# Optimization experiments

Hardware: AMD Instinct MI355X
Metric: run time of the kernel (lower is better)

The kernel has to match this reference:

```python
import jax, jax.numpy as jnp
import numpy as np

L, D, H, HD, FF, V, NH, S = 5, 1024, 8, 128, 4096, 2048, 15, 2
EPS = 1e-6
THETA = 10000.0


def rms_norm(x, w):
    x32 = x.astype(jnp.float32)
    y = x32 * jax.lax.rsqrt(jnp.mean(x32 * x32, axis=-1, keepdims=True) + EPS)
    return (y * w.astype(jnp.float32)).astype(x.dtype)


def rotate_half(x):
    x1, x2 = x[..., : HD // 2], x[..., HD // 2:]
    return jnp.concatenate((-x2, x1), axis=-1)


def setup_inputs() -> dict:
    key = jax.random.key(0)
    ks = jax.random.split(key, 20)
    s = 0.02
    inp = {
        "past_hidden": jax.random.normal(ks[0], (1, 1, D), jnp.float32),
        "cb0_token": jax.random.randint(ks[1], (1, 1), 0, V, jnp.int32),
        "codec_emb": jax.random.normal(ks[2], (V, D), jnp.float32) * s,
        "Wq": jax.random.normal(ks[3], (L, D, H * HD), jnp.float32) * s,
        "Wk": jax.random.normal(ks[4], (L, D, H * HD), jnp.float32) * s,
        "Wv": jax.random.normal(ks[5], (L, D, H * HD), jnp.float32) * s,
        "Wo": jax.random.normal(ks[6], (L, H * HD, D), jnp.float32) * s,
        "q_norm_w": jnp.ones((L, HD), jnp.float32),
        "k_norm_w": jnp.ones((L, HD), jnp.float32),
        "ln1_w": jnp.ones((L, D), jnp.float32),
        "ln2_w": jnp.ones((L, D), jnp.float32),
        "Wgate": jax.random.normal(ks[7], (L, D, FF), jnp.float32) * s,
        "Wup": jax.random.normal(ks[8], (L, D, FF), jnp.float32) * s,
        "Wdown": jax.random.normal(ks[9], (L, FF, D), jnp.float32) * s,
        "final_norm_w": jnp.ones((D,), jnp.float32),
        "lm_heads": jax.random.normal(ks[10], (NH, D, V), jnp.float32) * s,
    }
    return inp


def reference(past_hidden, codec_emb, Wq, Wk, Wv, Wo, q_norm_w, k_norm_w,
              ln1_w, ln2_w, Wgate, Wup, Wdown, final_norm_w, lm_heads,
              cb0_token):
    # Embed CB0 token and build 2-token prefill sequence [1, 2, D].
    cb0_embed = codec_emb[cb0_token]            # [1, 1, D]
    h = jnp.concatenate([past_hidden, cb0_embed], axis=1)

    # Rotary cos/sin for positions [0, 1]: [1, 1, S, HD].
    pos = jnp.arange(S, dtype=jnp.float32)
    inv_freq = 1.0 / (THETA ** (jnp.arange(0, HD, 2, dtype=jnp.float32) / HD))
    freqs = pos[:, None] * inv_freq[None, :]    # [S, HD/2]
    emb = jnp.concatenate([freqs, freqs], axis=-1)
    cos = jnp.cos(emb)[None, None]
    sin = jnp.sin(emb)[None, None]

    causal_mask = jnp.array([[0.0, -1e9], [0.0, 0.0]], jnp.float32)
    scale = 1.0 / np.sqrt(HD)

    def layer_step(h, p):
        wq, wk, wv, wo, qn, kn, l1, l2, wg, wu, wd = p
        res = h
        x = rms_norm(h, l1)                     # [1, S, D]
        q = (x @ wq).reshape(1, S, H, HD)
        k = (x @ wk).reshape(1, S, H, HD)
        v = (x @ wv).reshape(1, S, H, HD)
        q = rms_norm(q, qn)                     # per-head qk-norm
        k = rms_norm(k, kn)
        q = q.transpose(0, 2, 1, 3)             # [1, H, S, HD]
        k = k.transpose(0, 2, 1, 3)
        v = v.transpose(0, 2, 1, 3)
        q = q * cos + rotate_half(q) * sin
        k = k * cos + rotate_half(k) * sin
        attn = jnp.einsum('bhqd,bhkd->bhqk', q, k) * scale + causal_mask
        w = jax.nn.softmax(attn.astype(jnp.float32), axis=-1).astype(q.dtype)
        o = jnp.einsum('bhqk,bhkd->bhqd', w, v)
        o = o.transpose(0, 2, 1, 3).reshape(1, S, H * HD) @ wo
        h = res + o
        res = h
        x = rms_norm(h, l2)
        mlp = (jax.nn.silu(x @ wg) * (x @ wu)) @ wd
        return res + mlp, (k, v)

    h, (ks_, vs_) = jax.lax.scan(
        layer_step, h,
        (Wq, Wk, Wv, Wo, q_norm_w, k_norm_w, ln1_w, ln2_w, Wgate, Wup, Wdown))

    h = rms_norm(h, final_norm_w)
    last = h[:, -1, :]                          # [1, D]
    all_logits = jnp.einsum('bd,ndv->nbv', last, lm_heads)  # [15, 1, V]
    # Interleave keys/values per layer: [2L, 1, H, S, HD].
    kv_cache = jnp.stack([ks_, vs_], axis=1).reshape(2 * L, 1, H, S, HD)
    return all_logits, kv_cache
```

## Files before the change

### kernel.cpp

```cpp
#include <hip/hip_runtime.h>
#include <math.h>

#define EPS 1e-6f


__global__ void init_kernel(const float* __restrict__ past_hidden,
                            const float* __restrict__ codec_emb,
                            const int* __restrict__ tok,
                            float* __restrict__ ws,
                            float* __restrict__ logits)
{
    size_t idx = (size_t)blockIdx.x * blockDim.x + threadIdx.x;
    size_t stride = (size_t)gridDim.x * blockDim.x;
    for (size_t i = idx; i < 30720; i += stride) ws[2048 + i] = 0.f;
    for (size_t i = idx; i < 81920; i += stride) ws[43008 + i] = 0.f;
    for (size_t i = idx; i < 30720; i += stride) logits[i] = 0.f;
    int t = tok[0];
    for (size_t i = idx; i < 1024; i += stride) {
        ws[i]        = past_hidden[i];
        ws[1024 + i] = codec_emb[(size_t)t * 1024 + i];
    }
}

template <int S>
__global__ __launch_bounds__(256) void gemv_rms(
    const float* __restrict__ hbuf,
    const float* __restrict__ nw,
    const float* __restrict__ W0,
    const float* __restrict__ W1,
    const float* __restrict__ W2,
    size_t w_zstride,
    float* __restrict__ out,
    int out_sstride, int out_zstride,
    int D, int N)
{
    __shared__ float xs[S * 1024];
    __shared__ float red[S * 1024];
    __shared__ float tot[S];
    const int t = threadIdx.x;

    const float* W;
    if (W1) W = (blockIdx.z == 0) ? W0 : ((blockIdx.z == 1) ? W1 : W2);
    else    W = W0 + (size_t)blockIdx.z * w_zstride;
    float* outz = out + (size_t)blockIdx.z * out_zstride;

    if (nw) {
        float ss[S];
#pragma unroll
        for (int s = 0; s < S; ++s) ss[s] = 0.f;
        for (int dd = t; dd < D; dd += 256) {
#pragma unroll
            for (int s = 0; s < S; ++s) {
                float v = hbuf[s * D + dd];
                xs[s * 1024 + dd] = v;
                ss[s] += v * v;
            }
        }
#pragma unroll
        for (int s = 0; s < S; ++s) {
            red[t] = ss[s]; __syncthreads();
            for (int off = 128; off >= 1; off >>= 1) {
                if (t < off) red[t] += red[t + off];
                __syncthreads();
            }
            if (t == 0) tot[s] = red[0];
            __syncthreads();
        }
        float sc[S];
#pragma unroll
        for (int s = 0; s < S; ++s) sc[s] = rsqrtf(tot[s] / (float)D + EPS);
        for (int dd = t; dd < D; dd += 256) {
            float wv = nw[dd];
#pragma unroll
            for (int s = 0; s < S; ++s)
                xs[s * 1024 + dd] = xs[s * 1024 + dd] * sc[s] * wv;
        }
        __syncthreads();
    } else {
        for (int dd = t; dd < D; dd += 256) {
#pragma unroll
            for (int s = 0; s < S; ++s) xs[s * 1024 + dd] = hbuf[s * D + dd];
        }
        __syncthreads();
    }

    const int lane = t & 63;
    const int dp = t >> 6;
    const int j = blockIdx.x * 256 + lane * 4;
    const int d0 = blockIdx.y * 64 + dp * 16;

    float acc[S][4];
#pragma unroll
    for (int s = 0; s < S; ++s) { acc[s][0] = acc[s][1] = acc[s][2] = acc[s][3] = 0.f; }
#pragma unroll
    for (int i = 0; i < 16; ++i) {
        int dd = d0 + i;
        float4 w4 = *reinterpret_cast<const float4*>(W + (size_t)dd * N + j);
#pragma unroll
        for (int s = 0; s < S; ++s) {
            float xv = xs[s * 1024 + dd];
            acc[s][0] += xv * w4.x; acc[s][1] += xv * w4.y;
            acc[s][2] += xv * w4.z; acc[s][3] += xv * w4.w;
        }
    }
    __syncthreads();
#pragma unroll
    for (int s = 0; s < S; ++s)
#pragma unroll
        for (int c = 0; c < 4; ++c)
            red[(dp * S + s) * 256 + lane * 4 + c] = acc[s][c];
    __syncthreads();
    for (int o = t; o < S * 256; o += 256) {
        int s = o >> 8;
        int col = o & 255;
        float sum = 0.f;
#pragma unroll
        for (int dp2 = 0; dp2 < 4; ++dp2) sum += red[(dp2 * S + s) * 256 + col];
        atomicAdd(outz + (size_t)s * out_sstride + blockIdx.x * 256 + col, sum);
    }
}

__global__ void attn_kernel(const float* __restrict__ qkv,
                            const float* __restrict__ qnw,
                            const float* __restrict__ knw,
                            float* __restrict__ ao,
                            float* __restrict__ kvc)
{
    const int h = blockIdx.x;
    const int d = threadIdx.x;
    __shared__ float rbuf[128];
    __shared__ float qb[2][128], kb[2][128];

    float q[2], k[2], v[2];
#pragma unroll
    for (int s = 0; s < 2; ++s) {
        q[s] = qkv[s * 3072 +        h * 128 + d];
        k[s] = qkv[s * 3072 + 1024 + h * 128 + d];
        v[s] = qkv[s * 3072 + 2048 + h * 128 + d];
    }
    auto bred = [&](float val) -> float {
        rbuf[d] = val; __syncthreads();
        for (int off = 64; off >= 1; off >>= 1) {
            if (d < off) rbuf[d] += rbuf[d + off];
            __syncthreads();
        }
        float r = rbuf[0]; __syncthreads();
        return r;
    };
    float qs0 = bred(q[0] * q[0]);
    float qs1 = bred(q[1] * q[1]);
    float ks0 = bred(k[0] * k[0]);
    float ks1 = bred(k[1] * k[1]);
    float qsc[2] = { rsqrtf(qs0 / 128.f + EPS), rsqrtf(qs1 / 128.f + EPS) };
    float ksc[2] = { rsqrtf(ks0 / 128.f + EPS), rsqrtf(ks1 / 128.f + EPS) };
#pragma unroll
    for (int s = 0; s < 2; ++s) {
        qb[s][d] = q[s] * qsc[s] * qnw[d];
        kb[s][d] = k[s] * ksc[s] * knw[d];
    }
    __syncthreads();
    float invf = powf(10000.f, -(float)(d & 63) / 64.f);
    float qr[2], kr[2];
#pragma unroll
    for (int s = 0; s < 2; ++s) {
        float ang = (float)s * invf;
        float c = cosf(ang), si = sinf(ang);
        float qrot = (d < 64) ? -qb[s][d + 64] : qb[s][d - 64];
        float krot = (d < 64) ? -kb[s][d + 64] : kb[s][d - 64];
        qr[s] = qb[s][d] * c + qrot * si;
        kr[s] = kb[s][d] * c + krot * si;
    }
#pragma unroll
    for (int s = 0; s < 2; ++s) {
        kvc[h * 256 + s * 128 + d]        = kr[s];
        kvc[2048 + h * 256 + s * 128 + d] = v[s];
    }
    float p00 = bred(qr[0] * kr[0]);
    float p01 = bred(qr[0] * kr[1]);
    float p10 = bred(qr[1] * kr[0]);
    float p11 = bred(qr[1] * kr[1]);
    const float scale = 0.08838834764831845f;
    float s00 = p00 * scale, s01 = p01 * scale - 1e9f;
    float m0 = fmaxf(s00, s01);
    float e0 = expf(s00 - m0), e1 = expf(s01 - m0);
    float in0 = 1.f / (e0 + e1);
    float w00 = e0 * in0, w01 = e1 * in0;
    float s10 = p10 * scale, s11 = p11 * scale;
    float m1 = fmaxf(s10, s11);
    float f0 = expf(s10 - m1), f1 = expf(s11 - m1);
    float in1 = 1.f / (f0 + f1);
    float w10 = f0 * in1, w11 = f1 * in1;

    ao[0 * 1024 + h * 128 + d] = w00 * v[0] + w01 * v[1];
    ao[1 * 1024 + h * 128 + d] = w10 * v[0] + w11 * v[1];
}

__global__ __launch_bounds__(256) void gemv_down(
    const float* __restrict__ gu,
    const float* __restrict__ W,
    float* __restrict__ out)
{
    __shared__ float a[2][64];
    __shared__ float red[2048];
    const int t = threadIdx.x;
    const int d0 = blockIdx.y * 64;
    if (t < 128) {
        int s = t >> 6, f = d0 + (t & 63);
        float g = gu[s * 8192 + f];
        float u = gu[s * 8192 + 4096 + f];
        float sg = g / (1.f + expf(-g));
        a[s][t & 63] = sg * u;
    }
    __syncthreads();
    const int lane = t & 63;
    const int dp = t >> 6;
    const int j = blockIdx.x * 256 + lane * 4;
    float acc[2][4] = {{0.f,0.f,0.f,0.f},{0.f,0.f,0.f,0.f}};
#pragma unroll
    for (int i = 0; i < 16; ++i) {
        int dl = dp * 16 + i;
        int dd = d0 + dl;
        float4 w4 = *reinterpret_cast<const float4*>(W + (size_t)dd * 1024 + j);
#pragma unroll
        for (int s = 0; s < 2; ++s) {
            float xv = a[s][dl];
            acc[s][0] += xv * w4.x; acc[s][1] += xv * w4.y;
            acc[s][2] += xv * w4.z; acc[s][3] += xv * w4.w;
        }
    }
#pragma unroll
    for (int s = 0; s < 2; ++s)
#pragma unroll
        for (int c = 0; c < 4; ++c)
            red[(dp * 2 + s) * 256 + lane * 4 + c] = acc[s][c];
    __syncthreads();
    for (int o = t; o < 512; o += 256) {
        int s = o >> 8, col = o & 255;
        float sum = 0.f;
#pragma unroll
        for (int dp2 = 0; dp2 < 4; ++dp2) sum += red[(dp2 * 2 + s) * 256 + col];
        atomicAdd(out + s * 1024 + blockIdx.x * 256 + col, sum);
    }
}

__global__ void final_norm_kernel(const float* __restrict__ h,
                                  const float* __restrict__ w,
                                  float* __restrict__ outx)
{
    __shared__ float rbuf[256];
    __shared__ float tot;
    int t = threadIdx.x;
    float ss = 0.f;
    for (int dd = t; dd < 1024; dd += 256) { float v = h[1024 + dd]; ss += v * v; }
    rbuf[t] = ss; __syncthreads();
    for (int off = 128; off >= 1; off >>= 1) {
        if (t < off) rbuf[t] += rbuf[t + off];
        __syncthreads();
    }
    if (t == 0) tot = rbuf[0];
    __syncthreads();
    float sc = rsqrtf(tot / 1024.f + EPS);
    for (int dd = t; dd < 1024; dd += 256) outx[dd] = h[1024 + dd] * sc * w[dd];
}

extern "C" void kernel_launch(void* const* d_in, const int* in_sizes, int n_in,
                              void* d_out, int out_size, void* d_ws, size_t ws_size,
                              hipStream_t stream)
{
    const float* past_hidden = (const float*)d_in[0];
    const int*   cb0         = (const int*)d_in[1];
    const float* codec_emb   = (const float*)d_in[2];
    const float* Wq  = (const float*)d_in[3];
    const float* Wk  = (const float*)d_in[4];
    const float* Wv  = (const float*)d_in[5];
    const float* Wo  = (const float*)d_in[6];
    const float* qnw = (const float*)d_in[7];
    const float* knw = (const float*)d_in[8];
    const float* ln1 = (const float*)d_in[9];
    const float* ln2 = (const float*)d_in[10];
    const float* Wg  = (const float*)d_in[11];
    const float* Wu  = (const float*)d_in[12];
    const float* Wd  = (const float*)d_in[13];
    const float* fnw = (const float*)d_in[14];
    const float* lmh = (const float*)d_in[15];

    float* out = (float*)d_out;
    float* ws  = (float*)d_ws;
    float* h      = ws;
    float* qkvb   = ws + 2048;
    float* aob    = ws + 32768;
    float* gub    = ws + 43008;
    float* lastn  = ws + 124928;
    float* logits = out;
    float* kvc    = out + 30720;

    init_kernel<<<256, 256, 0, stream>>>(past_hidden, codec_emb, cb0, ws, logits);

    for (int l = 0; l < 5; ++l) {
        const float* wq = Wq + (size_t)l * 1024 * 1024;
        const float* wk = Wk + (size_t)l * 1024 * 1024;
        const float* wv = Wv + (size_t)l * 1024 * 1024;
        const float* wo = Wo + (size_t)l * 1024 * 1024;
        const float* wg = Wg + (size_t)l * 1024 * 4096;
        const float* wu = Wu + (size_t)l * 1024 * 4096;
        const float* wd = Wd + (size_t)l * 4096 * 1024;
        float* qkv = qkvb + (size_t)l * 6144;
        float* ao  = aob  + (size_t)l * 2048;
        float* gu  = gub  + (size_t)l * 16384;

        gemv_rms<2><<<dim3(4, 16, 3), 256, 0, stream>>>(
            h, ln1 + l * 1024, wq, wk, wv, 0, qkv, 3072, 1024, 1024, 1024);
        attn_kernel<<<8, 128, 0, stream>>>(qkv, qnw + l * 128, knw + l * 128, ao,
                                           kvc + (size_t)(2 * l) * 2048);
        gemv_rms<2><<<dim3(4, 16, 1), 256, 0, stream>>>(
            ao, nullptr, wo, nullptr, nullptr, 0, h, 1024, 0, 1024, 1024);
        gemv_rms<2><<<dim3(16, 16, 2), 256, 0, stream>>>(
            h, ln2 + l * 1024, wg, wu, wu, 0, gu, 8192, 4096, 1024, 4096);
        gemv_down<<<dim3(4, 64), 256, 0, stream>>>(gu, wd, h);
    }

    final_norm_kernel<<<1, 256, 0, stream>>>(h, fnw, lastn);
    gemv_rms<1><<<dim3(8, 16, 15), 256, 0, stream>>>(
        lastn, nullptr, lmh, nullptr, nullptr, (size_t)1024 * 2048,
        logits, 2048, 2048, 1024, 2048);
}
```

Measured before the change: 537.8 us.

## Fuse all layers into one persistent kernel with grid barriers and weight prefetch

Replaces the per-layer chain of separate kernel launches with a single persistent kernel of 256 workgroups that walks every layer stage, separated by atomic-counter grid barriers. Idle workgroups touch upcoming weight tiles to warm the cache while other stages run, and the attention step now writes into a zeroed buffer with atomics. This removes launch gaps and tail idle time, but relies on all 256 workgroups being co-resident and adds spin-barrier cost plus redundant prefetch loads.

```diff
diff --git a/kernel.cpp b/kernel.cpp
--- a/kernel.cpp
+++ b/kernel.cpp
@@ -2,7 +2,13 @@
 #include <math.h>
 
 #define EPS 1e-6f
-
+#define NWG 256
+
+#define WS_H    0
+#define WS_QKV  2048
+#define WS_AO   32768
+#define WS_GU   43008
+#define WS_CNT  126976
 
 __global__ void init_kernel(const float* __restrict__ past_hidden,
                             const float* __restrict__ codec_emb,
@@ -10,175 +16,193 @@
                             float* __restrict__ ws,
                             float* __restrict__ logits)
 {
-    size_t idx = (size_t)blockIdx.x * blockDim.x + threadIdx.x;
-    size_t stride = (size_t)gridDim.x * blockDim.x;
-    for (size_t i = idx; i < 30720; i += stride) ws[2048 + i] = 0.f;
-    for (size_t i = idx; i < 81920; i += stride) ws[43008 + i] = 0.f;
-    for (size_t i = idx; i < 30720; i += stride) logits[i] = 0.f;
+    int idx = blockIdx.x * blockDim.x + threadIdx.x;
+    int stride = gridDim.x * blockDim.x;
+    for (int i = idx; i < 30720; i += stride) ws[WS_QKV + i] = 0.f;
+    for (int i = idx; i < 10240; i += stride) ws[WS_AO + i] = 0.f;
+    for (int i = idx; i < 81920; i += stride) ws[WS_GU + i] = 0.f;
+    for (int i = idx; i < 30720; i += stride) logits[i] = 0.f;
+    for (int i = idx; i < 64; i += stride) ((unsigned*)(ws + WS_CNT))[i] = 0u;
     int t = tok[0];
-    for (size_t i = idx; i < 1024; i += stride) {
+    for (int i = idx; i < 1024; i += stride) {
         ws[i]        = past_hidden[i];
         ws[1024 + i] = codec_emb[(size_t)t * 1024 + i];
     }
 }
 
+__device__ __forceinline__ void gbar(unsigned* cnt, unsigned target)
+{
+    __threadfence();
+    __syncthreads();
+    if (threadIdx.x == 0) {
+        __hip_atomic_fetch_add(cnt, 1u, __ATOMIC_ACQ_REL, __HIP_MEMORY_SCOPE_AGENT);
+        while (__hip_atomic_load(cnt, __ATOMIC_RELAXED, __HIP_MEMORY_SCOPE_AGENT) < target) {
+            __builtin_amdgcn_s_sleep(2);
+        }
+    }
+    __syncthreads();
+    __threadfence();
+}
+
+__device__ __forceinline__ float wave_red64(float v)
+{
+    for (int o = 32; o >= 1; o >>= 1) v += __shfl_down(v, o, 64);
+    return v;
+}
+
+__device__ __forceinline__ void load_rms2(const float* __restrict__ h,
+                                          const float* __restrict__ nw,
+                                          float* __restrict__ x0, float* __restrict__ x1,
+                                          float* __restrict__ red)
+{
+    int t = threadIdx.x;
+    float ss0 = 0.f, ss1 = 0.f;
+    for (int d = t; d < 1024; d += 256) {
+        float v0 = h[d], v1 = h[1024 + d];
+        x0[d] = v0; x1[d] = v1;
+        ss0 += v0 * v0; ss1 += v1 * v1;
+    }
+    ss0 = wave_red64(ss0); ss1 = wave_red64(ss1);
+    if ((t & 63) == 0) { red[t >> 6] = ss0; red[4 + (t >> 6)] = ss1; }
+    __syncthreads();
+    float s0 = red[0] + red[1] + red[2] + red[3];
+    float s1 = red[4] + red[5] + red[6] + red[7];
+    float sc0 = rsqrtf(s0 / 1024.f + EPS);
+    float sc1 = rsqrtf(s1 / 1024.f + EPS);
+    __syncthreads();
+    for (int d = t; d < 1024; d += 256) {
+        float w = nw[d];
+        x0[d] *= sc0 * w; x1[d] *= sc1 * w;
+    }
+    __syncthreads();
+}
+
+__device__ __forceinline__ void load_rms1(const float* __restrict__ hrow,
+                                          const float* __restrict__ nw,
+                                          float* __restrict__ x,
+                                          float* __restrict__ red)
+{
+    int t = threadIdx.x;
+    float ss = 0.f;
+    for (int d = t; d < 1024; d += 256) { float v = hrow[d]; x[d] = v; ss += v * v; }
+    ss = wave_red64(ss);
+    if ((t & 63) == 0) red[t >> 6] = ss;
+    __syncthreads();
+    float s = red[0] + red[1] + red[2] + red[3];
+    float sc = rsqrtf(s / 1024.f + EPS);
+    __syncthreads();
+    for (int d = t; d < 1024; d += 256) x[d] *= sc * nw[d];
+    __syncthreads();
+}
+
 template <int S>
-__global__ __launch_bounds__(256) void gemv_rms(
-    const float* __restrict__ hbuf,
-    const float* __restrict__ nw,
-    const float* __restrict__ W0,
-    const float* __restrict__ W1,
-    const float* __restrict__ W2,
-    size_t w_zstride,
-    float* __restrict__ out,
-    int out_sstride, int out_zstride,
-    int D, int N)
-{
-    __shared__ float xs[S * 1024];
-    __shared__ float red[S * 1024];
-    __shared__ float tot[S];
-    const int t = threadIdx.x;
-
-    const float* W;
-    if (W1) W = (blockIdx.z == 0) ? W0 : ((blockIdx.z == 1) ? W1 : W2);
-    else    W = W0 + (size_t)blockIdx.z * w_zstride;
-    float* outz = out + (size_t)blockIdx.z * out_zstride;
-
-    if (nw) {
-        float ss[S];
-#pragma unroll
-        for (int s = 0; s < S; ++s) ss[s] = 0.f;
-        for (int dd = t; dd < D; dd += 256) {
-#pragma unroll
-            for (int s = 0; s < S; ++s) {
-                float v = hbuf[s * D + dd];
-                xs[s * 1024 + dd] = v;
-                ss[s] += v * v;
-            }
-        }
-#pragma unroll
-        for (int s = 0; s < S; ++s) {
-            red[t] = ss[s]; __syncthreads();
-            for (int off = 128; off >= 1; off >>= 1) {
-                if (t < off) red[t] += red[t + off];
-                __syncthreads();
-            }
-            if (t == 0) tot[s] = red[0];
-            __syncthreads();
-        }
-        float sc[S];
-#pragma unroll
-        for (int s = 0; s < S; ++s) sc[s] = rsqrtf(tot[s] / (float)D + EPS);
-        for (int dd = t; dd < D; dd += 256) {
-            float wv = nw[dd];
-#pragma unroll
-            for (int s = 0; s < S; ++s)
-                xs[s * 1024 + dd] = xs[s * 1024 + dd] * sc[s] * wv;
-        }
-        __syncthreads();
-    } else {
-        for (int dd = t; dd < D; dd += 256) {
-#pragma unroll
-            for (int s = 0; s < S; ++s) xs[s * 1024 + dd] = hbuf[s * D + dd];
-        }
-        __syncthreads();
-    }
-
-    const int lane = t & 63;
-    const int dp = t >> 6;
-    const int j = blockIdx.x * 256 + lane * 4;
-    const int d0 = blockIdx.y * 64 + dp * 16;
-
-    float acc[S][4];
-#pragma unroll
-    for (int s = 0; s < S; ++s) { acc[s][0] = acc[s][1] = acc[s][2] = acc[s][3] = 0.f; }
+__device__ __forceinline__ void task_gemm(const float* __restrict__ x0,
+                                          const float* __restrict__ x1,
+                                          const float* __restrict__ Wt, int N,
+                                          float* __restrict__ o0, float* __restrict__ o1,
+                                          float* __restrict__ red)
+{
+    const int t = threadIdx.x, lane = t & 63, dp = t >> 6;
+    const float* Wp = Wt + (size_t)(dp * 16) * N + lane * 4;
+    const float* xa = x0 + dp * 16;
+    const float* xb = (S == 2) ? (x1 + dp * 16) : nullptr;
+    float a0 = 0.f, a1 = 0.f, a2 = 0.f, a3 = 0.f;
+    float b0 = 0.f, b1 = 0.f, b2 = 0.f, b3 = 0.f;
 #pragma unroll
     for (int i = 0; i < 16; ++i) {
-        int dd = d0 + i;
-        float4 w4 = *reinterpret_cast<const float4*>(W + (size_t)dd * N + j);
+        float4 w = *reinterpret_cast<const float4*>(Wp + (size_t)i * N);
+        float xv = xa[i];
+        a0 += xv * w.x; a1 += xv * w.y; a2 += xv * w.z; a3 += xv * w.w;
+        if (S == 2) {
+            float yv = xb[i];
+            b0 += yv * w.x; b1 += yv * w.y; b2 += yv * w.z; b3 += yv * w.w;
+        }
+    }
+    __syncthreads();
+    red[(dp * S + 0) * 256 + lane * 4 + 0] = a0;
+    red[(dp * S + 0) * 256 + lane * 4 + 1] = a1;
+    red[(dp * S + 0) * 256 + lane * 4 + 2] = a2;
+    red[(dp * S + 0) * 256 + lane * 4 + 3] = a3;
+    if (S == 2) {
+        red[(dp * S + 1) * 256 + lane * 4 + 0] = b0;
+        red[(dp * S + 1) * 256 + lane * 4 + 1] = b1;
+        red[(dp * S + 1) * 256 + lane * 4 + 2] = b2;
+        red[(dp * S + 1) * 256 + lane * 4 + 3] = b3;
+    }
+    __syncthreads();
+    for (int o = t; o < S * 256; o += 256) {
+        int s = o >> 8, col = o & 255;
+        float sum = red[(0 * S + s) * 256 + col] + red[(1 * S + s) * 256 + col]
+                  + red[(2 * S + s) * 256 + col] + red[(3 * S + s) * 256 + col];
+        atomicAdd(((s == 0) ? o0 : o1) + col, sum);
+    }
+}
+
+__device__ __forceinline__ float touch_tile(const float* __restrict__ Wt, int N)
+{
+    const int t = threadIdx.x, lane = t & 63, dp = t >> 6;
+    const float* Wp = Wt + (size_t)(dp * 16) * N + lane * 4;
+    float s = 0.f;
 #pragma unroll
-        for (int s = 0; s < S; ++s) {
-            float xv = xs[s * 1024 + dd];
-            acc[s][0] += xv * w4.x; acc[s][1] += xv * w4.y;
-            acc[s][2] += xv * w4.z; acc[s][3] += xv * w4.w;
-        }
-    }
-    __syncthreads();
-#pragma unroll
-    for (int s = 0; s < S; ++s)
-#pragma unroll
-        for (int c = 0; c < 4; ++c)
-            red[(dp * S + s) * 256 + lane * 4 + c] = acc[s][c];
-    __syncthreads();
-    for (int o = t; o < S * 256; o += 256) {
-        int s = o >> 8;
-        int col = o & 255;
-        float sum = 0.f;
-#pragma unroll
-        for (int dp2 = 0; dp2 < 4; ++dp2) sum += red[(dp2 * S + s) * 256 + col];
-        atomicAdd(outz + (size_t)s * out_sstride + blockIdx.x * 256 + col, sum);
-    }
-}
-
-__global__ void attn_kernel(const float* __restrict__ qkv,
-                            const float* __restrict__ qnw,
-                            const float* __restrict__ knw,
-                            float* __restrict__ ao,
-                            float* __restrict__ kvc)
-{
-    const int h = blockIdx.x;
-    const int d = threadIdx.x;
-    __shared__ float rbuf[128];
-    __shared__ float qb[2][128], kb[2][128];
-
-    float q[2], k[2], v[2];
-#pragma unroll
-    for (int s = 0; s < 2; ++s) {
-        q[s] = qkv[s * 3072 +        h * 128 + d];
-        k[s] = qkv[s * 3072 + 1024 + h * 128 + d];
-        v[s] = qkv[s * 3072 + 2048 + h * 128 + d];
+    for (int i = 0; i < 16; ++i) {
+        float4 w = *reinterpret_cast<const float4*>(Wp + (size_t)i * N);
+        s += w.x + w.y + w.z + w.w;
+    }
+    return s;
+}
+
+__device__ void attn_head(const float* __restrict__ qkv,
+                          const float* __restrict__ qnw, const float* __restrict__ knw,
+                          float* __restrict__ ao, float* __restrict__ kvc,
+                          int head, float* __restrict__ red)
+{
+    const int t = threadIdx.x;
+    const int d = t & 127;
+    const bool act = t < 128;
+    float q0 = 0.f, q1 = 0.f, k0 = 0.f, k1 = 0.f, v0 = 0.f, v1 = 0.f, qw = 0.f, kw = 0.f;
+    if (act) {
+        q0 = qkv[head * 128 + d];           q1 = qkv[3072 + head * 128 + d];
+        k0 = qkv[1024 + head * 128 + d];    k1 = qkv[3072 + 1024 + head * 128 + d];
+        v0 = qkv[2048 + head * 128 + d];    v1 = qkv[3072 + 2048 + head * 128 + d];
+        qw = qnw[d]; kw = knw[d];
     }
     auto bred = [&](float val) -> float {
-        rbuf[d] = val; __syncthreads();
-        for (int off = 64; off >= 1; off >>= 1) {
-            if (d < off) rbuf[d] += rbuf[d + off];
+        red[t] = act ? val : 0.f; __syncthreads();
+        for (int off = 128; off >= 1; off >>= 1) {
+            if (t < off) red[t] += red[t + off];
             __syncthreads();
         }
-        float r = rbuf[0]; __syncthreads();
+        float r = red[0]; __syncthreads();
         return r;
     };
-    float qs0 = bred(q[0] * q[0]);
-    float qs1 = bred(q[1] * q[1]);
-    float ks0 = bred(k[0] * k[0]);
-    float ks1 = bred(k[1] * k[1]);
-    float qsc[2] = { rsqrtf(qs0 / 128.f + EPS), rsqrtf(qs1 / 128.f + EPS) };
-    float ksc[2] = { rsqrtf(ks0 / 128.f + EPS), rsqrtf(ks1 / 128.f + EPS) };
-#pragma unroll
-    for (int s = 0; s < 2; ++s) {
-        qb[s][d] = q[s] * qsc[s] * qnw[d];
-        kb[s][d] = k[s] * ksc[s] * knw[d];
-    }
-    __syncthreads();
-    float invf = powf(10000.f, -(float)(d & 63) / 64.f);
-    float qr[2], kr[2];
-#pragma unroll
-    for (int s = 0; s < 2; ++s) {
-        float ang = (float)s * invf;
-        float c = cosf(ang), si = sinf(ang);
-        float qrot = (d < 64) ? -qb[s][d + 64] : qb[s][d - 64];
-        float krot = (d < 64) ? -kb[s][d + 64] : kb[s][d - 64];
-        qr[s] = qb[s][d] * c + qrot * si;
-        kr[s] = kb[s][d] * c + krot * si;
-    }
-#pragma unroll
-    for (int s = 0; s < 2; ++s) {
-        kvc[h * 256 + s * 128 + d]        = kr[s];
-        kvc[2048 + h * 256 + s * 128 + d] = v[s];
-    }
-    float p00 = bred(qr[0] * kr[0]);
-    float p01 = bred(qr[0] * kr[1]);
-    float p10 = bred(qr[1] * kr[0]);
-    float p11 = bred(qr[1] * kr[1]);
+    float qs0 = bred(q0 * q0), qs1 = bred(q1 * q1);
+    float ks0 = bred(k0 * k0), ks1 = bred(k1 * k1);
+    float qsc0 = rsqrtf(qs0 / 128.f + EPS), qsc1 = rsqrtf(qs1 / 128.f + EPS);
+    float ksc0 = rsqrtf(ks0 / 128.f + EPS), ksc1 = rsqrtf(ks1 / 128.f + EPS);
+    float* qb = red + 256;
+    float* kb = red + 512;
+    if (act) {
+        qb[d] = q0 * qsc0 * qw; qb[128 + d] = q1 * qsc1 * qw;
+        kb[d] = k0 * ksc0 * kw; kb[128 + d] = k1 * ksc1 * kw;
+    }
+    __syncthreads();
+    float qr0 = 0.f, qr1 = 0.f, kr0 = 0.f, kr1 = 0.f;
+    if (act) {
+        float invf = powf(10000.f, -(float)(d & 63) / 64.f);
+        qr0 = qb[d];
+        kr0 = kb[d];
+        float c = cosf(invf), si = sinf(invf);
+        float qrot = (d < 64) ? -qb[128 + d + 64] : qb[128 + d - 64];
+        float krot = (d < 64) ? -kb[128 + d + 64] : kb[128 + d - 64];
+        qr1 = qb[128 + d] * c + qrot * si;
+        kr1 = kb[128 + d] * c + krot * si;
+        kvc[head * 256 + d]              = kr0;
+        kvc[head * 256 + 128 + d]        = kr1;
+        kvc[2048 + head * 256 + d]       = v0;
+        kvc[2048 + head * 256 + 128 + d] = v1;
+    }
+    float p00 = bred(qr0 * kr0), p01 = bred(qr0 * kr1);
+    float p10 = bred(qr1 * kr0), p11 = bred(qr1 * kr1);
     const float scale = 0.08838834764831845f;
     float s00 = p00 * scale, s01 = p01 * scale - 1e9f;
     float m0 = fmaxf(s00, s01);
@@ -190,77 +214,145 @@
     float f0 = expf(s10 - m1), f1 = expf(s11 - m1);
     float in1 = 1.f / (f0 + f1);
     float w10 = f0 * in1, w11 = f1 * in1;
-
-    ao[0 * 1024 + h * 128 + d] = w00 * v[0] + w01 * v[1];
-    ao[1 * 1024 + h * 128 + d] = w10 * v[0] + w11 * v[1];
-}
-
-__global__ __launch_bounds__(256) void gemv_down(
-    const float* __restrict__ gu,
-    const float* __restrict__ W,
-    float* __restrict__ out)
-{
-    __shared__ float a[2][64];
+    if (act) {
+        atomicAdd(ao + head * 128 + d,        w00 * v0 + w01 * v1);
+        atomicAdd(ao + 1024 + head * 128 + d, w10 * v0 + w11 * v1);
+    }
+}
+
+__global__ __launch_bounds__(256) void mega_kernel(
+    const float* __restrict__ Wq, const float* __restrict__ Wk, const float* __restrict__ Wv,
+    const float* __restrict__ Wo,
+    const float* __restrict__ qnw_all, const float* __restrict__ knw_all,
+    const float* __restrict__ ln1_all, const float* __restrict__ ln2_all,
+    const float* __restrict__ Wg, const float* __restrict__ Wu, const float* __restrict__ Wd,
+    const float* __restrict__ fnw, const float* __restrict__ lmh,
+    float* __restrict__ ws, float* __restrict__ logits, float* __restrict__ kvc_all)
+{
+    __shared__ float xs0[1024];
+    __shared__ float xs1[1024];
     __shared__ float red[2048];
-    const int t = threadIdx.x;
-    const int d0 = blockIdx.y * 64;
-    if (t < 128) {
-        int s = t >> 6, f = d0 + (t & 63);
-        float g = gu[s * 8192 + f];
-        float u = gu[s * 8192 + 4096 + f];
-        float sg = g / (1.f + expf(-g));
-        a[s][t & 63] = sg * u;
-    }
-    __syncthreads();
-    const int lane = t & 63;
-    const int dp = t >> 6;
-    const int j = blockIdx.x * 256 + lane * 4;
-    float acc[2][4] = {{0.f,0.f,0.f,0.f},{0.f,0.f,0.f,0.f}};
-#pragma unroll
-    for (int i = 0; i < 16; ++i) {
-        int dl = dp * 16 + i;
-        int dd = d0 + dl;
-        float4 w4 = *reinterpret_cast<const float4*>(W + (size_t)dd * 1024 + j);
-#pragma unroll
-        for (int s = 0; s < 2; ++s) {
-            float xv = a[s][dl];
-            acc[s][0] += xv * w4.x; acc[s][1] += xv * w4.y;
-            acc[s][2] += xv * w4.z; acc[s][3] += xv * w4.w;
-        }
-    }
-#pragma unroll
-    for (int s = 0; s < 2; ++s)
-#pragma unroll
-        for (int c = 0; c < 4; ++c)
-            red[(dp * 2 + s) * 256 + lane * 4 + c] = acc[s][c];
-    __syncthreads();
-    for (int o = t; o < 512; o += 256) {
-        int s = o >> 8, col = o & 255;
-        float sum = 0.f;
-#pragma unroll
-        for (int dp2 = 0; dp2 < 4; ++dp2) sum += red[(dp2 * 2 + s) * 256 + col];
-        atomicAdd(out + s * 1024 + blockIdx.x * 256 + col, sum);
-    }
-}
-
-__global__ void final_norm_kernel(const float* __restrict__ h,
-                                  const float* __restrict__ w,
-                                  float* __restrict__ outx)
-{
-    __shared__ float rbuf[256];
-    __shared__ float tot;
-    int t = threadIdx.x;
-    float ss = 0.f;
-    for (int dd = t; dd < 1024; dd += 256) { float v = h[1024 + dd]; ss += v * v; }
-    rbuf[t] = ss; __syncthreads();
-    for (int off = 128; off >= 1; off >>= 1) {
-        if (t < off) rbuf[t] += rbuf[t + off];
-        __syncthreads();
-    }
-    if (t == 0) tot = rbuf[0];
-    __syncthreads();
-    float sc = rsqrtf(tot / 1024.f + EPS);
-    for (int dd = t; dd < 1024; dd += 256) outx[dd] = h[1024 + dd] * sc * w[dd];
+    const int wg = blockIdx.x;
+    unsigned* cnt = (unsigned*)(ws + WS_CNT);
+    unsigned target = 0;
+    float* h = ws + WS_H;
+    float sink = 0.f;
+
+    for (int l = 0; l < 5; ++l) {
+        const float* wq_ = Wq + (size_t)l * 1048576;
+        const float* wk_ = Wk + (size_t)l * 1048576;
+        const float* wv_ = Wv + (size_t)l * 1048576;
+        const float* wo_ = Wo + (size_t)l * 1048576;
+        const float* wg_ = Wg + (size_t)l * 4194304;
+        const float* wu_ = Wu + (size_t)l * 4194304;
+        const float* wd_ = Wd + (size_t)l * 4194304;
+        float* qkv = ws + WS_QKV + l * 6144;
+        float* ao  = ws + WS_AO  + l * 2048;
+        float* gu  = ws + WS_GU  + l * 16384;
+
+        load_rms2(h, ln1_all + l * 1024, xs0, xs1, red);
+        if (wg < 192) {
+            int z = wg >> 6, r = wg & 63, jb = r >> 4, kb = r & 15;
+            const float* Wz = (z == 0) ? wq_ : ((z == 1) ? wk_ : wv_);
+            task_gemm<2>(&xs0[kb * 64], &xs1[kb * 64],
+                         Wz + (size_t)(kb * 64) * 1024 + jb * 256, 1024,
+                         qkv + z * 1024 + jb * 256, qkv + 3072 + z * 1024 + jb * 256, red);
+        }
+        if (wg < 64) {
+            int jb = wg >> 4, kb = wg & 15;
+            sink += touch_tile(wo_ + (size_t)(kb * 64) * 1024 + jb * 256, 1024);
+        } else {
+            int jb = wg >> 4, kb = wg & 15;
+            sink += touch_tile(wg_ + (size_t)(kb * 64) * 4096 + jb * 256, 4096);
+        }
+        target += NWG; gbar(cnt, target);
+
+        if (wg < 8)
+            attn_head(qkv, qnw_all + l * 128, knw_all + l * 128, ao,
+                      kvc_all + (size_t)(2 * l) * 2048, wg, red);
+        if (wg < 64) {
+            int jb = wg >> 4, kb = wg & 15;
+            sink += touch_tile(wg_ + (size_t)(kb * 64) * 4096 + jb * 256, 4096);
+        }
+        target += NWG; gbar(cnt, target);
+
+        {
+            int t = threadIdx.x;
+            for (int d2 = t; d2 < 1024; d2 += 256) { xs0[d2] = ao[d2]; xs1[d2] = ao[1024 + d2]; }
+            __syncthreads();
+        }
+        if (wg < 64) {
+            int jb = wg >> 4, kb = wg & 15;
+            task_gemm<2>(&xs0[kb * 64], &xs1[kb * 64],
+                         wo_ + (size_t)(kb * 64) * 1024 + jb * 256, 1024,
+                         h + jb * 256, h + 1024 + jb * 256, red);
+        }
+        {
+            int jb = wg >> 4, kb = wg & 15;
+            sink += touch_tile(wu_ + (size_t)(kb * 64) * 4096 + jb * 256, 4096);
+        }
+        target += NWG; gbar(cnt, target);
+
+        load_rms2(h, ln2_all + l * 1024, xs0, xs1, red);
+        {
+            int jb = wg >> 4, kb = wg & 15;
+            task_gemm<2>(&xs0[kb * 64], &xs1[kb * 64],
+                         wg_ + (size_t)(kb * 64) * 4096 + jb * 256, 4096,
+                         gu + jb * 256, gu + 8192 + jb * 256, red);
+            task_gemm<2>(&xs0[kb * 64], &xs1[kb * 64],
+                         wu_ + (size_t)(kb * 64) * 4096 + jb * 256, 4096,
+                         gu + 4096 + jb * 256, gu + 8192 + 4096 + jb * 256, red);
+            int jb2 = wg >> 6, kb2 = wg & 63;
+            sink += touch_tile(wd_ + (size_t)(kb2 * 64) * 1024 + jb2 * 256, 1024);
+        }
+        target += NWG; gbar(cnt, target);
+
+        {
+            int jb = wg >> 6, kb = wg & 63;
+            int t = threadIdx.x;
+            if (t < 128) {
+                int s = t >> 6, f = kb * 64 + (t & 63);
+                float g = gu[s * 8192 + f];
+                float u = gu[s * 8192 + 4096 + f];
+                xs0[t & 63 + 0] = 0.f;
+            }
+            __syncthreads();
+            if (t < 128) {
+                int s = t >> 6, f = kb * 64 + (t & 63);
+                float g = gu[s * 8192 + f];
+                float u = gu[s * 8192 + 4096 + f];
+                float a = (g / (1.f + expf(-g))) * u;
+                if (s == 0) xs0[t & 63] = a; else xs1[t & 63] = a;
+            }
+            __syncthreads();
+            task_gemm<2>(&xs0[0], &xs1[0],
+                         wd_ + (size_t)(kb * 64) * 1024 + jb * 256, 1024,
+                         h + jb * 256, h + 1024 + jb * 256, red);
+            if (l < 4) {
+                if (wg < 192) {
+                    int z = wg >> 6, r = wg & 63, jb3 = r >> 4, kb3 = r & 15;
+                    const float* nq = (z == 0) ? (Wq + (size_t)(l + 1) * 1048576)
+                                   : ((z == 1) ? (Wk + (size_t)(l + 1) * 1048576)
+                                               : (Wv + (size_t)(l + 1) * 1048576));
+                    sink += touch_tile(nq + (size_t)(kb3 * 64) * 1024 + jb3 * 256, 1024);
+                }
+            } else {
+                int n = wg >> 7, r = wg & 127, jb3 = r >> 4, kb3 = r & 15;
+                sink += touch_tile(lmh + (size_t)n * 2097152 + (size_t)(kb3 * 64) * 2048 + jb3 * 256, 2048);
+            }
+        }
+        target += NWG; gbar(cnt, target);
+    }
+
+    load_rms1(h + 1024, fnw, xs0, red);
+    for (int task = wg; task < 1920; task += NWG) {
+        int n = task >> 7, r = task & 127, jb = r >> 4, kb = r & 15;
+        task_gemm<1>(&xs0[kb * 64], nullptr,
+                     lmh + (size_t)n * 2097152 + (size_t)(kb * 64) * 2048 + jb * 256, 2048,
+                     logits + n * 2048 + jb * 256, nullptr, red);
+    }
+
+    if (sink == -1.2345e38f) atomicAdd(h, 1.0f);
 }
 
 extern "C" void kernel_launch(void* const* d_in, const int* in_sizes, int n_in,
@@ -284,43 +376,12 @@
     const float* fnw = (const float*)d_in[14];
     const float* lmh = (const float*)d_in[15];
 
-    float* out = (float*)d_out;
-    float* ws  = (float*)d_ws;
-    float* h      = ws;
-    float* qkvb   = ws + 2048;
-    float* aob    = ws + 32768;
-    float* gub    = ws + 43008;
-    float* lastn  = ws + 124928;
+    float* out    = (float*)d_out;
+    float* ws     = (float*)d_ws;
     float* logits = out;
     float* kvc    = out + 30720;
 
-    init_kernel<<<256, 256, 0, stream>>>(past_hidden, codec_emb, cb0, ws, logits);
-
-    for (int l = 0; l < 5; ++l) {
-        const float* wq = Wq + (size_t)l * 1024 * 1024;
-        const float* wk = Wk + (size_t)l * 1024 * 1024;
-        const float* wv = Wv + (size_t)l * 1024 * 1024;
-        const float* wo = Wo + (size_t)l * 1024 * 1024;
-        const float* wg = Wg + (size_t)l * 1024 * 4096;
-        const float* wu = Wu + (size_t)l * 1024 * 4096;
-        const float* wd = Wd + (size_t)l * 4096 * 1024;
-        float* qkv = qkvb + (size_t)l * 6144;
-        float* ao  = aob  + (size_t)l * 2048;
-        float* gu  = gub  + (size_t)l * 16384;
-
-        gemv_rms<2><<<dim3(4, 16, 3), 256, 0, stream>>>(
-            h, ln1 + l * 1024, wq, wk, wv, 0, qkv, 3072, 1024, 1024, 1024);
-        attn_kernel<<<8, 128, 0, stream>>>(qkv, qnw + l * 128, knw + l * 128, ao,
-                                           kvc + (size_t)(2 * l) * 2048);
-        gemv_rms<2><<<dim3(4, 16, 1), 256, 0, stream>>>(
-            ao, nullptr, wo, nullptr, nullptr, 0, h, 1024, 0, 1024, 1024);
-        gemv_rms<2><<<dim3(16, 16, 2), 256, 0, stream>>>(
-            h, ln2 + l * 1024, wg, wu, wu, 0, gu, 8192, 4096, 1024, 4096);
-        gemv_down<<<dim3(4, 64), 256, 0, stream>>>(gu, wd, h);
-    }
-
-    final_norm_kernel<<<1, 256, 0, stream>>>(h, fnw, lastn);
-    gemv_rms<1><<<dim3(8, 16, 15), 256, 0, stream>>>(
-        lastn, nullptr, lmh, nullptr, nullptr, (size_t)1024 * 2048,
-        logits, 2048, 2048, 1024, 2048);
-}
+    init_kernel<<<128, 256, 0, stream>>>(past_hidden, codec_emb, cb0, ws, logits);
+    mega_kernel<<<NWG, 256, 0, stream>>>(Wq, Wk, Wv, Wo, qnw, knw, ln1, ln2,
+                                         Wg, Wu, Wd, fnw, lmh, ws, logits, kvc);
+}
```

Measured after the change: 2.060 ms. +283.1%, slower.
